# Kernel optimization log

Measured on AMD Instinct MI355X. Metric: run time of the kernel, lower is better.

The kernel has to match this reference:

```python
import jax, jax.numpy as jnp
import numpy as np
from math import factorial

N_SCALES = 4
K_ORI = 4
NA = 9


def _grids(h, w):
    fy = (jnp.arange(h) - h // 2) * (2.0 / h)
    fx = (jnp.arange(w) - w // 2) * (2.0 / w)
    FY, FX = jnp.meshgrid(fy, fx, indexing='ij')
    r = jnp.sqrt(FX ** 2 + FY ** 2)
    r = jnp.where(r == 0, 1.0 / max(h, w), r)
    return jnp.log2(r), jnp.arctan2(FY, FX)


def _rc_hi(lr, lo, hi):
    # sqrt raised-cosine rising 0->1 over log_rad in [lo, hi]
    t = jnp.clip((lr - lo) / (hi - lo), 0.0, 1.0)
    return jnp.sqrt(0.5 * (1.0 - jnp.cos(jnp.pi * t)))


def _rc_lo(lr, lo, hi):
    t = jnp.clip((lr - lo) / (hi - lo), 0.0, 1.0)
    return jnp.sqrt(0.5 * (1.0 + jnp.cos(jnp.pi * t)))


def _angle_masks(angle, K, is_complex):
    order = K - 1
    const = (2.0 ** (2 * order)) * (factorial(order) ** 2) / (K * factorial(2 * order))
    masks = []
    for b in range(K):
        d = jnp.mod(angle - jnp.pi * b / K + jnp.pi, 2 * jnp.pi) - jnp.pi
        if is_complex:  # single-sided (analytic) mask
            m = 2.0 * np.sqrt(const) * (jnp.cos(d) ** order) * (jnp.abs(d) < jnp.pi / 2)
        else:
            m = np.sqrt(const) * (jnp.cos(d) ** order)
        masks.append(m)
    return masks


def _build_pyramid(img, n_scales, K):
    # complex steerable pyramid in the frequency domain (tight_frame=False)
    order = K - 1
    h, w = img.shape
    imdft = jnp.fft.fftshift(jnp.fft.fft2(img))
    lr, ang = _grids(h, w)
    hi0 = _rc_hi(lr, -1.0, 0.0)
    lo0 = _rc_lo(lr, -1.0, 0.0)
    coeffs = {'residual_highpass': jnp.real(jnp.fft.ifft2(jnp.fft.ifftshift(imdft * hi0)))}
    lodft = imdft * lo0
    cph = (-1j) ** order
    for s in range(n_scales):
        hh, ww = lodft.shape
        lr, ang = _grids(hh, ww)
        him = _rc_hi(lr, -2.0, -1.0)
        for b, am in enumerate(_angle_masks(ang, K, True)):
            coeffs[(s, b)] = jnp.fft.ifft2(jnp.fft.ifftshift(cph * lodft * him * am))
        # spectral crop = spatial downsample by 2, then lowpass
        lodft = lodft[hh // 4: hh // 4 + hh // 2, ww // 4: ww // 4 + ww // 2]
        lr2, _ = _grids(hh // 2, ww // 2)
        lodft = lodft * _rc_lo(lr2, -1.0, 0.0)
    coeffs['residual_lowpass'] = jnp.real(jnp.fft.ifft2(jnp.fft.ifftshift(lodft)))
    return coeffs


def _lo0_filter(im):
    # height-0 pyramid residual lowpass == lo0 filtering (filterPyr in the torch code)
    h, w = im.shape
    lr, _ = _grids(h, w)
    return jnp.real(jnp.fft.ifft2(jnp.fft.ifftshift(jnp.fft.fftshift(jnp.fft.fft2(im)) * _rc_lo(lr, -1.0, 0.0))))


def _expand(im, f=2):
    # frequency-domain upsampling by factor f (Portilla_Simoncelli.expand)
    h, w = im.shape
    dft = jnp.fft.fftshift(jnp.fft.fft2(im)).astype(jnp.complex64)
    big = jnp.zeros((f * h, f * w), dtype=jnp.complex64)
    big = big.at[(f * h - h) // 2:(f * h - h) // 2 + h, (f * w - w) // 2:(f * w - w) // 2 + w].set(dft)
    return jnp.fft.ifft2(jnp.fft.ifftshift(big)) * (f * f)


def _recon_band(real_bands, K):
    # recon_pyr(levels=[0]) of a height-1 real pyramid whose bands were replaced
    order = K - 1
    h, w = real_bands[0].shape
    lr, ang = _grids(h, w)
    lo0 = _rc_lo(lr, -1.0, 0.0)
    him = _rc_hi(lr, -2.0, -1.0)
    ph = (1j) ** order
    recondft = jnp.zeros((h, w), dtype=jnp.complex64)
    for b, am in enumerate(_angle_masks(ang, K, False)):
        recondft = recondft + ph * jnp.fft.fftshift(jnp.fft.fft2(real_bands[b])) * him * am
    return jnp.real(jnp.fft.ifft2(jnp.fft.ifftshift(recondft * lo0)))


def _autocorr(ch, la):
    h, w = ch.shape
    F = jnp.fft.fft2(ch)
    ac = jnp.fft.fftshift(jnp.real(jnp.fft.ifft2(jnp.abs(F) ** 2))) / (h * w)
    cx, cy = h // 2, w // 2
    le = int(min(min(h, w) / 2 - 1, la))
    return ac[cx - le:cx + le + 1, cy - le:cy + le + 1], ac[cx, cy], le


def _skew_kurt(ch, vari, var0):
    cond = (vari / var0) > 1e-6
    skew = jnp.where(cond, jnp.mean(ch ** 3) / (vari ** 1.5), 0.0)
    kurt = jnp.where(cond, jnp.mean(ch ** 4) / (vari ** 2), 3.0)
    return skew, kurt


def _ps_forward(image):
    n_scales, K, Na = N_SCALES, K_ORI, NA
    img = image.reshape(image.shape[-2], image.shape[-1])
    mu = jnp.mean(img)
    var0 = jnp.var(img, ddof=1)
    cimg = img - mu
    pix = jnp.stack([mu, var0,
                     jnp.mean(cimg ** 3) / (var0 ** 1.5),
                     jnp.mean(cimg ** 4) / (var0 ** 2),
                     jnp.min(img), jnp.max(img)])
    coeffs = _build_pyramid(img, n_scales, K)
    coeffs['residual_lowpass'] = coeffs['residual_lowpass'] - jnp.mean(coeffs['residual_lowpass'])
    keys = ['residual_highpass'] + [(s, b) for s in range(n_scales) for b in range(K)] + ['residual_lowpass']
    mag, realc, mag_means = {}, {}, []
    for kk in keys:
        v = coeffs[kk]
        m = jnp.abs(v)
        mm = jnp.mean(m)
        mag_means.append(mm)
        mag[kk] = m - mm
        realc[kk] = jnp.real(v)
    mag_means = jnp.stack(mag_means)
    la = (Na - 1) // 2
    auto_corr = jnp.zeros((Na, Na, n_scales + 1))
    acm = jnp.zeros((Na, Na, n_scales, K))
    skew_r = jnp.zeros((n_scales + 1,))
    kurt_r = jnp.zeros((n_scales + 1,))
    recon = _lo0_filter(coeffs['residual_lowpass'])
    patch, vari, le = _autocorr(recon, la)
    auto_corr = auto_corr.at[la - le:la + le + 1, la - le:la + le + 1, n_scales].set(patch)
    sk, ku = _skew_kurt(recon, vari, var0)
    skew_r = skew_r.at[n_scales].set(sk)
    kurt_r = kurt_r.at[n_scales].set(ku)
    for s in range(n_scales - 1, -1, -1):
        for b in range(K):
            patch, vari, le = _autocorr(mag[(s, b)], la)
            acm = acm.at[la - le:la + le + 1, la - le:la + le + 1, s, b].set(patch)
        recon = jnp.real(_expand(recon, 2) / 4.0)
        recon = recon + _recon_band([realc[(s, b)] for b in range(K)], K)
        patch, vari, le = _autocorr(recon, la)
        auto_corr = auto_corr.at[la - le:la + le + 1, la - le:la + le + 1, s].set(patch)
        sk, ku = _skew_kurt(recon, vari, var0)
        skew_r = skew_r.at[s].set(sk)
        kurt_r = kurt_r.at[s].set(ku)
    K2 = max(2 * K, 5)
    coc_mag = jnp.zeros((K, K, n_scales + 1))
    csc_mag = jnp.zeros((K, K, n_scales))
    coc_real = jnp.zeros((K2, K2, n_scales + 1))
    csc_real = jnp.zeros((2 * K, K2, n_scales))
    for s in range(n_scales):
        hs, ws = realc[(s, 0)].shape
        csz = hs * ws
        if s < n_scales - 1:
            pars, rpr, rpi = [], [], []
            for b in range(K):
                tmp = _expand(coeffs[(s + 1, b)], 2) / 4.0
                rt, it = jnp.real(tmp), jnp.imag(tmp)
                mg = jnp.sqrt(rt ** 2 + it ** 2)
                a2 = 2.0 * jnp.arctan2(rt, it)  # note arg order matches torch code
                rpr.append((mg * jnp.cos(a2)).T.reshape(-1))
                rpi.append((mg * jnp.sin(a2)).T.reshape(-1))
                pars.append((mg - jnp.mean(mg)).T.reshape(-1))
            parents = jnp.stack(pars, 1)
            rparents = jnp.stack(rpr + rpi, 1)
        else:
            tmp = jnp.real(_expand(coeffs['residual_lowpass'], 2) / 4.0).T
            rparents = jnp.stack([tmp.reshape(-1),
                                  jnp.roll(tmp, 1, 0).reshape(-1),
                                  jnp.roll(tmp, -1, 0).reshape(-1),
                                  jnp.roll(tmp, 1, 1).reshape(-1),
                                  jnp.roll(tmp, -1, 1).reshape(-1)], 1)
            parents = None
        cousins = jnp.stack([mag[(s, b)].T.reshape(-1) for b in range(K)], 1)
        coc_mag = coc_mag.at[:, :, s].set(cousins.T @ cousins / csz)
        if parents is not None:
            csc_mag = csc_mag.at[:, :, s].set(cousins.T @ parents / csz)
        rcousins = jnp.stack([realc[(s, b)].T.reshape(-1) for b in range(K)], 1)
        coc_real = coc_real.at[:K, :K, s].set(rcousins.T @ rcousins / csz)
        nrp = rparents.shape[1]
        csc_real = csc_real.at[:K, :nrp, s].set(rcousins.T @ rparents / csz)
        if s == n_scales - 1:
            coc_real = coc_real.at[:nrp, :nrp, n_scales].set(rparents.T @ rparents / (csz / 4.0))
    var_hp = jnp.mean(coeffs['residual_highpass'] ** 2)
    return jnp.concatenate([pix, mag_means, acm.reshape(-1), skew_r, kurt_r,
                            auto_corr.reshape(-1), coc_mag.reshape(-1), csc_mag.reshape(-1),
                            coc_real.reshape(-1), csc_real.reshape(-1), var_hp.reshape(1)])


def setup_inputs() -> dict:
    key = jax.random.key(0)
    image = jax.random.normal(key, (1, 1, 1024, 1024), dtype=jnp.float32)
    return {"image": image}


def reference(image):
    return _ps_forward(image)
```

## Files before the change

### kernel.cpp

```cpp
#include <hip/hip_runtime.h>
#include <math.h>

typedef float2 cplx;

#define PI_F 3.14159265358979323846f
#define SQC  0.8944271909999159f

#define GS_FOR(i, n) for (int i = blockIdx.x * blockDim.x + threadIdx.x; i < (n); i += gridDim.x * blockDim.x)
#define RED_GRID 256

__device__ __forceinline__ float ufreq(int i, int n) {
  return (float)((i < (n >> 1)) ? i : i - n) * (2.0f / (float)n);
}
__device__ __forceinline__ void grid_lr_ang(int i, int j, int n, float* lr, float* ang) {
  float fy = ufreq(i, n), fx = ufreq(j, n);
  float r = sqrtf(fx * fx + fy * fy);
  if (i == 0 && j == 0) r = 1.0f / (float)n;
  *lr = log2f(r);
  *ang = atan2f(fy, fx);
}
__device__ __forceinline__ float rc_hi_f(float lr, float lo, float hi) {
  float t = (lr - lo) / (hi - lo);
  t = fminf(fmaxf(t, 0.0f), 1.0f);
  return sqrtf(0.5f * (1.0f - cosf(PI_F * t)));
}
__device__ __forceinline__ float rc_lo_f(float lr, float lo, float hi) {
  float t = (lr - lo) / (hi - lo);
  t = fminf(fmaxf(t, 0.0f), 1.0f);
  return sqrtf(0.5f * (1.0f + cosf(PI_F * t)));
}
__device__ __forceinline__ float wrap_d(float ang, int b) {
  float d = ang - PI_F * (float)b * 0.25f + PI_F;
  d = d - floorf(d * (0.5f / PI_F)) * (2.0f * PI_F);
  return d - PI_F;
}
__device__ __forceinline__ float amask_c(float ang, int b) {
  float d = wrap_d(ang, b);
  float c = cosf(d);
  float m = 2.0f * SQC * c * c * c;
  return (fabsf(d) < 0.5f * PI_F) ? m : 0.0f;
}
__device__ __forceinline__ float amask_r(float ang, int b) {
  float d = wrap_d(ang, b);
  float c = cosf(d);
  return SQC * c * c * c;
}

__device__ __forceinline__ double wred_d(double v) {
#pragma unroll
  for (int o = 32; o > 0; o >>= 1) v += __shfl_down(v, o);
  return v;
}
template<int NS>
__device__ __forceinline__ void block_to_parts(double* __restrict__ part, int slotBase, double* v) {
  __shared__ double lds[NS][4];
  const int wid = threadIdx.x >> 6, lane = threadIdx.x & 63;
#pragma unroll
  for (int q = 0; q < NS; ++q) {
    double r = wred_d(v[q]);
    if (lane == 0) lds[q][wid] = r;
  }
  __syncthreads();
  for (int q = threadIdx.x; q < NS; q += blockDim.x) {
    double s = lds[q][0] + lds[q][1] + lds[q][2] + lds[q][3];
    part[(size_t)(slotBase + q) * RED_GRID + blockIdx.x] = s;
  }
}
__global__ void reduce_parts_k(double* __restrict__ acc, const double* __restrict__ part, int base) {
  const double* p = part + (size_t)(base + blockIdx.x) * RED_GRID;
  double s = 0;
  for (int i = threadIdx.x; i < RED_GRID; i += 64) s += p[i];
  s = wred_d(s);
  if (threadIdx.x == 0) acc[base + blockIdx.x] = s;
}
__device__ __forceinline__ void atomicMinF(float* a, float v) {
  if (v >= 0.0f) atomicMin((int*)a, __float_as_int(v));
  else atomicMax((unsigned int*)a, __float_as_uint(v));
}
__device__ __forceinline__ void atomicMaxF(float* a, float v) {
  if (v >= 0.0f) atomicMax((int*)a, __float_as_int(v));
  else atomicMin((unsigned int*)a, __float_as_uint(v));
}

template<int LOGN, bool INV>
__global__ __launch_bounds__(256) void fft_rows_k(cplx* __restrict__ d) {
  constexpr int N = 1 << LOGN;
  __shared__ cplx sh[N];
  __shared__ cplx tw[N / 2];
  const int tid = threadIdx.x;
  const int T = blockDim.x;
  cplx* rp = d + (size_t)blockIdx.x * N;
  for (int k = tid; k < N / 2; k += T) {
    float a = (INV ? 2.0f : -2.0f) * PI_F * (float)k / (float)N;
    float s, c;
    sincosf(a, &s, &c);
    tw[k] = make_float2(c, s);
  }
  for (int i = tid; i < N; i += T) {
    unsigned r = __brev((unsigned)i) >> (32 - LOGN);
    sh[r] = rp[i];
  }
  __syncthreads();
  for (int len = 2; len <= N; len <<= 1) {
    const int half = len >> 1;
    const int tstep = N / len;
    for (int j = tid; j < N / 2; j += T) {
      int pos = j & (half - 1);
      int base = (j - pos) << 1;
      cplx w = tw[pos * tstep];
      cplx a = sh[base + pos];
      cplx b = sh[base + pos + half];
      float tx = b.x * w.x - b.y * w.y;
      float ty = b.x * w.y + b.y * w.x;
      sh[base + pos] = make_float2(a.x + tx, a.y + ty);
      sh[base + pos + half] = make_float2(a.x - tx, a.y - ty);
    }
    __syncthreads();
  }
  const float sc = INV ? (1.0f / (float)N) : 1.0f;
  for (int i = tid; i < N; i += T) {
    cplx v = sh[i];
    rp[i] = make_float2(v.x * sc, v.y * sc);
  }
}

__global__ void transpose_k(cplx* __restrict__ out, const cplx* __restrict__ in, int N) {
  __shared__ cplx tile[32][33];
  size_t po = (size_t)blockIdx.z * N * N;
  int bx = blockIdx.x * 32, by = blockIdx.y * 32;
  int x = bx + threadIdx.x;
  for (int dy = threadIdx.y; dy < 32; dy += 8)
    tile[dy][threadIdx.x] = in[po + (size_t)(by + dy) * N + x];
  __syncthreads();
  int xo = by + threadIdx.x;
  for (int dy = threadIdx.y; dy < 32; dy += 8)
    out[po + (size_t)(bx + dy) * N + xo] = tile[threadIdx.x][dy];
}

__global__ void r2c_k(cplx* out, const float* in, int n) {
  GS_FOR(i, n) out[i] = make_float2(in[i], 0.0f);
}
__global__ void hp_lo_split_k(cplx* hp, cplx* lod, const cplx* spec, int logN) {
  int N = 1 << logN, n = N * N;
  GS_FOR(idx, n) {
    int i = idx >> logN, j = idx & (N - 1);
    float lr, ang;
    grid_lr_ang(i, j, N, &lr, &ang);
    float h0 = rc_hi_f(lr, -1.0f, 0.0f);
    float l0 = rc_lo_f(lr, -1.0f, 0.0f);
    cplx z = spec[idx];
    hp[idx]  = make_float2(z.x * h0, z.y * h0);
    lod[idx] = make_float2(z.x * l0, z.y * l0);
  }
}
__global__ void rhp_stats_k(const cplx* src, int n, double* part) {
  double sa = 0, sq = 0;
  GS_FOR(i, n) {
    float v = src[i].x;
    sa += fabsf(v);
    sq += (double)v * (double)v;
  }
  double v[2] = {sa, sq};
  block_to_parts<2>(part, 4, v);
}
__global__ void band_spec_k(cplx* out, const cplx* lod, int logN, int b0, int P) {
  int N = 1 << logN, n = N * N;
  GS_FOR(idx, n) {
    int i = idx >> logN, j = idx & (N - 1);
    float lr, ang;
    grid_lr_ang(i, j, N, &lr, &ang);
    float him = rc_hi_f(lr, -2.0f, -1.0f);
    cplx z = lod[idx];
    for (int p = 0; p < P; ++p) {
      float m = him * amask_c(ang, b0 + p);
      out[p * n + idx] = make_float2(-z.y * m, z.x * m);
    }
  }
}
template<int P>
__global__ void extract_band_k(float* realc, float* mag, const cplx* src, int logPer,
                               double* part, int slotBase) {
  int n = (1 << logPer) * P;
  double s0 = 0, s1 = 0, s2 = 0, s3 = 0;
  GS_FOR(idx, n) {
    cplx z = src[idx];
    float m = sqrtf(z.x * z.x + z.y * z.y);
    realc[idx] = z.x;
    mag[idx] = m;
    int p = idx >> logPer;
    if (p == 0) s0 += m; else if (p == 1) s1 += m; else if (p == 2) s2 += m; else s3 += m;
  }
  double v[4] = {s0, s1, s2, s3};
  block_to_parts<P>(part, slotBase, v);
}
__global__ void center_k(float* buf, int logPer, int P, const double* acc0) {
  int nPer = 1 << logPer, n = nPer * P;
  double inv = 1.0 / (double)nPer;
  GS_FOR(idx, n) buf[idx] -= (float)(acc0[idx >> logPer] * inv);
}
__global__ void lod_down_k(cplx* child, const cplx* par, int logNc) {
  int Nc = 1 << logNc, n = Nc * Nc, Np = Nc << 1;
  GS_FOR(idx, n) {
    int i = idx >> logNc, j = idx & (Nc - 1);
    int pi = (i < (Nc >> 1)) ? i : i + Nc;
    int pj = (j < (Nc >> 1)) ? j : j + Nc;
    float lr, ang;
    grid_lr_ang(i, j, Nc, &lr, &ang);
    float l0 = rc_lo_f(lr, -1.0f, 0.0f);
    cplx z = par[pi * Np + pj];
    child[idx] = make_float2(z.x * l0, z.y * l0);
  }
}
__global__ void sum_real2_k(const cplx* src, int n, double* part) {
  double s = 0;
  GS_FOR(i, n) s += (double)src[i].x;
  double v[1] = {s};
  block_to_parts<1>(part, 24, v);
}
__global__ void center_abs2_k(const cplx* src, int n, const double* acc, double* part) {
  float mu = (float)(acc[24] / (double)n);
  double s = 0;
  GS_FOR(i, n) s += fabsf(src[i].x - mu);
  double v[1] = {s};
  block_to_parts<1>(part, 25, v);
}
__global__ void rs4_init_k(cplx* rs, const cplx* lod4) {
  GS_FOR(idx, 4096) {
    int i = idx >> 6, j = idx & 63;
    float lr, ang;
    grid_lr_ang(i, j, 64, &lr, &ang);
    float l0 = rc_lo_f(lr, -1.0f, 0.0f);
    cplx v = lod4[idx];
    if (idx == 0) v = make_float2(0.0f, 0.0f);
    rs[idx] = make_float2(v.x * l0, v.y * l0);
  }
}
__global__ void embed_rs_k(cplx* dst, const cplx* src, int logNb, int zeroDC) {
  int Nb = 1 << logNb, Nc = Nb >> 1, q = Nc >> 1, n = Nb * Nb;
  GS_FOR(idx, n) {
    int i = idx >> logNb, j = idx & (Nb - 1);
    int ci = (i < q) ? i : ((i >= Nb - q) ? (i - Nb + Nc) : -1);
    int cj = (j < q) ? j : ((j >= Nb - q) ? (j - Nb + Nc) : -1);
    cplx v = make_float2(0.0f, 0.0f);
    if (ci >= 0 && cj >= 0) {
      v = src[ci * Nc + cj];
      if (zeroDC && ci == 0 && cj == 0) v = make_float2(0.0f, 0.0f);
    }
    dst[idx] = v;
  }
}
__global__ void recon_step_k(cplx* __restrict__ dst, const cplx* __restrict__ src,
                             const cplx* __restrict__ lod, int logNb) {
  int Nb = 1 << logNb, Nc = Nb >> 1, qq = Nc >> 1, n = Nb * Nb;
  GS_FOR(idx, n) {
    int i = idx >> logNb, j = idx & (Nb - 1);
    int ci = (i < qq) ? i : ((i >= Nb - qq) ? (i - Nb + Nc) : -1);
    int cj = (j < qq) ? j : ((j >= Nb - qq) ? (j - Nb + Nc) : -1);
    float ex = 0.0f, ey = 0.0f;
    if (ci >= 0 && cj >= 0) { cplx v = src[ci * Nc + cj]; ex = v.x; ey = v.y; }
    int ni = (Nb - i) & (Nb - 1), nj = (Nb - j) & (Nb - 1);
    float lr, ang;
    grid_lr_ang(i, j, Nb, &lr, &ang);
    float him = rc_hi_f(lr, -2.0f, -1.0f);
    float l0 = rc_lo_f(lr, -1.0f, 0.0f);
    cplx L = lod[idx];
    cplx L2 = lod[ni * Nb + nj];
    float sx = 0.0f, sy = 0.0f;
#pragma unroll
    for (int b = 0; b < 4; ++b) {
      float c1 = him * amask_c(ang, b);
      float c2 = him * amask_c(ang + PI_F, b);
      float mr = him * amask_r(ang, b);
      float gx = L.x * c1 - L2.x * c2;
      float gy = L.y * c1 + L2.y * c2;
      sx += 0.5f * mr * gx;
      sy += 0.5f * mr * gy;
    }
    dst[idx] = make_float2(ex + sx * l0, ey + sy * l0);
  }
}
__global__ void embed_band_k(cplx* dst, const cplx* lodc, int logNb, int b0, int P) {
  int Nb = 1 << logNb, Nc = Nb >> 1, q = Nc >> 1, n = Nb * Nb;
  int tot = n * P;
  GS_FOR(idxAll, tot) {
    int p = idxAll >> (2 * logNb);
    int idx = idxAll & (n - 1);
    int i = idx >> logNb, j = idx & (Nb - 1);
    int ci = (i < q) ? i : ((i >= Nb - q) ? (i - Nb + Nc) : -1);
    int cj = (j < q) ? j : ((j >= Nb - q) ? (j - Nb + Nc) : -1);
    cplx v = make_float2(0.0f, 0.0f);
    if (ci >= 0 && cj >= 0) {
      float lr, ang;
      grid_lr_ang(ci, cj, Nc, &lr, &ang);
      float m = rc_hi_f(lr, -2.0f, -1.0f) * amask_c(ang, b0 + p);
      cplx z = lodc[ci * Nc + cj];
      v = make_float2(-z.y * m, z.x * m);
    }
    dst[idxAll] = v;
  }
}
template<int ST, bool SK>
__device__ __forceinline__ void ac_core(const float* __restrict__ xp, int logN,
                                        double* __restrict__ part, int slotBase) {
  const int N = 1 << logN;
  const int nu = (N * N) >> 3;
  float acc[41];
#pragma unroll
  for (int q = 0; q < 41; ++q) acc[q] = 0.0f;
  float a3 = 0.0f, a4 = 0.0f;
  for (int u = blockIdx.x * blockDim.x + threadIdx.x; u < nu; u += gridDim.x * blockDim.x) {
    int i = u >> (logN - 3);
    int j0 = (u & ((N >> 3) - 1)) << 3;
    float buf[5][16];
#pragma unroll
    for (int di = 0; di < 5; ++di) {
      int r = ((i + di) & (N - 1)) << logN;
#pragma unroll
      for (int blk = 0; blk < 4; ++blk) {
        int c = (j0 - 4 + blk * 4) & (N - 1);
        if (ST == 1) {
          const float4 v = *reinterpret_cast<const float4*>(xp + r + c);
          buf[di][blk * 4 + 0] = v.x; buf[di][blk * 4 + 1] = v.y;
          buf[di][blk * 4 + 2] = v.z; buf[di][blk * 4 + 3] = v.w;
        } else {
          const float4 v0 = *reinterpret_cast<const float4*>(xp + ((size_t)(r + c) << 1));
          const float4 v1 = *reinterpret_cast<const float4*>(xp + ((size_t)(r + c) << 1) + 4);
          buf[di][blk * 4 + 0] = v0.x; buf[di][blk * 4 + 1] = v0.z;
          buf[di][blk * 4 + 2] = v1.x; buf[di][blk * 4 + 3] = v1.z;
        }
      }
    }
#pragma unroll
    for (int k = 0; k < 8; ++k) {
      float xc = buf[0][4 + k];
      if (SK) {
        float x2 = xc * xc;
        a3 += x2 * xc;
        a4 += x2 * x2;
      }
#pragma unroll
      for (int q = 0; q < 41; ++q) {
        const int di = (q < 5) ? 0 : 1 + (q - 5) / 9;
        const int dj = (q < 5) ? q : ((q - 5) % 9) - 4;
        acc[q] += xc * buf[di][4 + k + dj];
      }
    }
  }
  constexpr int NS = SK ? 43 : 41;
  double v[NS];
#pragma unroll
  for (int q = 0; q < 41; ++q) v[q] = (double)acc[q];
  if (SK) { v[41] = (double)a3; v[42] = (double)a4; }
  block_to_parts<NS>(part, slotBase, v);
}
__global__ __launch_bounds__(256) void acm_vec_k(const float* m0, const float* m1,
                                                 const float* m2, const float* m3, double* part) {
  const int s = blockIdx.z;
  const float* base = (s == 0) ? m0 : ((s == 1) ? m1 : ((s == 2) ? m2 : m3));
  const int logN = 10 - s;
  const float* xp = base + ((size_t)blockIdx.y << (2 * logN));
  ac_core<1, false>(xp, logN, part, 448 + (s * 4 + blockIdx.y) * 41);
}
__global__ __launch_bounds__(256) void ac_rec_k(const float* x, int logN, double* part, int slotBase) {
  ac_core<2, true>(x, logN, part, slotBase);
}
__global__ void img_stats1_k(const float* img, int n, double* part, float* mm) {
  double s = 0;
  float mn = INFINITY, mx = -INFINITY;
  GS_FOR(i, n) {
    float v = img[i];
    s += (double)v;
    mn = fminf(mn, v);
    mx = fmaxf(mx, v);
  }
  double v[1] = {s};
  block_to_parts<1>(part, 0, v);
#pragma unroll
  for (int o = 32; o > 0; o >>= 1) {
    mn = fminf(mn, __shfl_down(mn, o));
    mx = fmaxf(mx, __shfl_down(mx, o));
  }
  if ((threadIdx.x & 63) == 0) {
    atomicMinF(mm + 0, mn);
    atomicMaxF(mm + 1, mx);
  }
}
__global__ void img_stats2_k(const float* img, int n, const double* acc, double* part) {
  double mu = acc[0] / (double)n;
  double s2 = 0, s3 = 0, s4 = 0;
  GS_FOR(i, n) {
    double c = (double)img[i] - mu;
    double c2 = c * c;
    s2 += c2;
    s3 += c2 * c;
    s4 += c2 * c2;
  }
  double v[3] = {s2, s3, s4};
  block_to_parts<3>(part, 1, v);
}
template<bool WS>
__global__ void gram4_k(const float* base, int n, double* part, int slotBase) {
  constexpr int NS = WS ? 20 : 16;
  double g[16];
  double s[4];
#pragma unroll
  for (int q = 0; q < 16; ++q) g[q] = 0;
#pragma unroll
  for (int q = 0; q < 4; ++q) s[q] = 0;
  GS_FOR(i, n) {
    double d0 = base[i], d1 = base[n + i], d2 = base[2 * n + i], d3 = base[3 * n + i];
    g[0] += d0 * d0; g[1] += d0 * d1; g[2]  += d0 * d2; g[3]  += d0 * d3;
    g[5] += d1 * d1; g[6] += d1 * d2; g[7]  += d1 * d3;
    g[10] += d2 * d2; g[11] += d2 * d3;
    g[15] += d3 * d3;
    if (WS) { s[0] += d0; s[1] += d1; s[2] += d2; s[3] += d3; }
  }
  g[4] = g[1]; g[8] = g[2]; g[12] = g[3]; g[9] = g[6]; g[13] = g[7]; g[14] = g[11];
  double v[NS];
#pragma unroll
  for (int q = 0; q < 16; ++q) v[q] = g[q];
  if (WS) {
#pragma unroll
    for (int q = 0; q < 4; ++q) v[16 + q] = s[q];
  }
  block_to_parts<NS>(part, slotBase, v);
}
__global__ void parent_reduce_k(const cplx* par, const float* magS, const float* realS, int n,
                                double* part, int slotBase) {
  double d[13];
#pragma unroll
  for (int q = 0; q < 13; ++q) d[q] = 0;
  GS_FOR(i, n) {
    cplx z = par[i];
    float rt = z.x, it = z.y;
    float mg = sqrtf(rt * rt + it * it);
    float rpr = 0.0f, rpi = 0.0f;
    if (mg > 0.0f) {
      rpr = (it * it - rt * rt) / mg;
      rpi = 2.0f * rt * it / mg;
    }
    d[0] += (double)mg;
#pragma unroll
    for (int b = 0; b < 4; ++b) d[1 + b] += (double)magS[b * n + i] * (double)mg;
#pragma unroll
    for (int b = 0; b < 4; ++b) {
      double rv = (double)realS[b * n + i];
      d[5 + b] += rv * (double)rpr;
      d[9 + b] += rv * (double)rpi;
    }
  }
  block_to_parts<13>(part, slotBase, d);
}
__global__ void lp_parent2_k(const cplx* X, const float* realS, int logN, double* part) {
  int N = 1 << logN, n = N * N;
  double d[45];
#pragma unroll
  for (int q = 0; q < 45; ++q) d[q] = 0;
  GS_FOR(idx, n) {
    int i = idx >> logN, j = idx & (N - 1);
    float c[5];
    c[0] = X[idx].x;
    c[1] = X[i * N + ((j - 1) & (N - 1))].x;
    c[2] = X[i * N + ((j + 1) & (N - 1))].x;
    c[3] = X[((i - 1) & (N - 1)) * N + j].x;
    c[4] = X[((i + 1) & (N - 1)) * N + j].x;
#pragma unroll
    for (int b = 0; b < 4; ++b) {
      double rv = (double)realS[b * n + idx];
#pragma unroll
      for (int k = 0; k < 5; ++k) d[b * 5 + k] += rv * (double)c[k];
    }
#pragma unroll
    for (int a = 0; a < 5; ++a)
#pragma unroll
      for (int k = 0; k < 5; ++k) d[20 + a * 5 + k] += (double)c[a] * (double)c[k];
  }
  block_to_parts<45>(part, 370, d);
}
__global__ void init_mm_k(float* mm) {
  if (threadIdx.x == 0) { mm[0] = INFINITY; mm[1] = -INFINITY; }
}

__global__ void assemble_k(float* out, const double* acc, const float* mm) {
  const int t = threadIdx.x;
  const double NPIX = 1048576.0;
  double var0 = acc[1] / (NPIX - 1.0);
  if (t == 0) {
    double mu = acc[0] / NPIX;
    out[0] = (float)mu;
    out[1] = (float)var0;
    out[2] = (float)((acc[2] / NPIX) / pow(var0, 1.5));
    out[3] = (float)((acc[3] / NPIX) / (var0 * var0));
    out[4] = mm[0];
    out[5] = mm[1];
    out[2455] = (float)(acc[5] / NPIX);
  }
  for (int k = t; k < 18; k += blockDim.x) {
    double n, sv;
    if (k == 0) { n = NPIX; sv = acc[4]; }
    else if (k == 17) { n = 4096.0; sv = acc[25]; }
    else { int s = (k - 1) >> 2; double dd = (double)(1024 >> s); n = dd * dd; sv = acc[7 + k]; }
    out[6 + k] = (float)(sv / n);
  }
  for (int si = t; si < 5; si += blockDim.x) {
    double dd = (si == 4) ? 64.0 : (double)(1024 >> si);
    double nn = dd * dd;
    double vari = acc[1104 + si * 43] / nn;
    bool cond = (vari / var0) > 1e-6;
    double m3 = acc[1104 + si * 43 + 41] / nn, m4 = acc[1104 + si * 43 + 42] / nn;
    out[1320 + si] = (float)(cond ? m3 / pow(vari, 1.5) : 0.0);
    out[1325 + si] = (float)(cond ? m4 / (vari * vari) : 3.0);
  }
  for (int w = t; w < 656; w += blockDim.x) {
    int patch = w / 41, q = w - patch * 41;
    int s = patch >> 2, b = patch & 3;
    double dd = (double)(1024 >> s);
    double v = acc[448 + w] / (dd * dd);
    int di = (q < 5) ? 0 : 1 + (q - 5) / 9;
    int dj = (q < 5) ? q : ((q - 5) % 9) - 4;
    int pi = 4 + di, pj = 4 + dj;
    out[24 + 144 * pi + 16 * pj + 4 * s + b] = (float)v;
    if (q) out[24 + 144 * (8 - pi) + 16 * (8 - pj) + 4 * s + b] = (float)v;
  }
  for (int w = t; w < 205; w += blockDim.x) {
    int si = w / 41, q = w - si * 41;
    double dd = (si == 4) ? 64.0 : (double)(1024 >> si);
    double v = acc[1104 + si * 43 + q] / (dd * dd);
    int di = (q < 5) ? 0 : 1 + (q - 5) / 9;
    int dj = (q < 5) ? q : ((q - 5) % 9) - 4;
    int pi = 4 + di, pj = 4 + dj;
    out[1330 + (pi * 9 + pj) * 5 + si] = (float)v;
    if (q) out[1330 + ((8 - pi) * 9 + (8 - pj)) * 5 + si] = (float)v;
  }
  for (int q = t; q < 64; q += blockDim.x) {
    int s = q >> 4, ij = q & 15;
    double dd = (double)(1024 >> s); double csz = dd * dd;
    out[1735 + ij * 5 + s] = (float)(acc[64 + s * 20 + ij] / csz);
  }
  for (int q = t; q < 64; q += blockDim.x) {
    int s = q >> 4, ij = q & 15;
    int i = ij >> 2, j = ij & 3;
    double dd = (double)(1024 >> s); double csz = dd * dd;
    out[1879 + (i * 8 + j) * 5 + s] = (float)(acc[144 + s * 16 + ij] / csz);
  }
  for (int q = t; q < 25; q += blockDim.x) {
    int a = q / 5, b2 = q - a * 5;
    out[1879 + (a * 8 + b2) * 5 + 4] = (float)(acc[390 + q] / 4096.0);
  }
  for (int q = t; q < 48; q += blockDim.x) {
    int s = q >> 4, ij = q & 15;
    int i = ij >> 2, pb = ij & 3;
    double dd = (double)(1024 >> s); double csz = dd * dd;
    const double* ps = acc + 208 + (s * 4 + pb) * 13;
    double meanp = ps[0] / csz;
    double cousSum = acc[64 + s * 20 + 16 + i];
    out[1815 + (i * 4 + pb) * 4 + s] = (float)((ps[1 + i] - meanp * cousSum) / csz);
  }
  for (int q = t; q < 96; q += blockDim.x) {
    int s = q >> 5, r = q & 31;
    int i = r >> 3, j = r & 7;
    int pb = j & 3, offq = (j >= 4) ? 9 : 5;
    double dd = (double)(1024 >> s); double csz = dd * dd;
    out[2199 + (i * 8 + j) * 4 + s] = (float)(acc[208 + (s * 4 + pb) * 13 + offq + i] / csz);
  }
  for (int q = t; q < 20; q += blockDim.x) {
    int i = q / 5, c = q - i * 5;
    out[2199 + (i * 8 + c) * 4 + 3] = (float)(acc[370 + q] / 16384.0);
  }
}

static void fft_rows(cplx* d, int N, int rows, bool inv, hipStream_t st) {
  dim3 g(rows);
  int T = (N >= 512) ? 256 : ((N == 256) ? 128 : 64);
  dim3 b(T);
  switch (N) {
    case 64:   if (inv) fft_rows_k<6,  true><<<g, b, 0, st>>>(d); else fft_rows_k<6,  false><<<g, b, 0, st>>>(d); break;
    case 128:  if (inv) fft_rows_k<7,  true><<<g, b, 0, st>>>(d); else fft_rows_k<7,  false><<<g, b, 0, st>>>(d); break;
    case 256:  if (inv) fft_rows_k<8,  true><<<g, b, 0, st>>>(d); else fft_rows_k<8,  false><<<g, b, 0, st>>>(d); break;
    case 512:  if (inv) fft_rows_k<9,  true><<<g, b, 0, st>>>(d); else fft_rows_k<9,  false><<<g, b, 0, st>>>(d); break;
    case 1024: if (inv) fft_rows_k<10, true><<<g, b, 0, st>>>(d); else fft_rows_k<10, false><<<g, b, 0, st>>>(d); break;
    default: break;
  }
}
static void fft2d(cplx* a, cplx* b, int N, int P, bool inv, hipStream_t st) {
  fft_rows(a, N, N * P, inv, st);
  dim3 tg(N / 32, N / 32, P), tb(32, 8);
  transpose_k<<<tg, tb, 0, st>>>(b, a, N);
  fft_rows(b, N, N * P, inv, st);
  transpose_k<<<tg, tb, 0, st>>>(a, b, N);
}
static inline dim3 gsz(int n) {
  int b = (n + 255) >> 8;
  if (b > 2048) b = 2048;
  if (b < 1) b = 1;
  return dim3(b);
}

extern "C" void kernel_launch(void* const* d_in, const int* in_sizes, int n_in,
                              void* d_out, int out_size, void* d_ws, size_t ws_size,
                              hipStream_t stream) {
  (void)in_sizes; (void)n_in; (void)out_size; (void)ws_size;
  const float* img = (const float*)d_in[0];
  float* out = (float*)d_out;

  char* wsb = (char*)d_ws;
  size_t off = 0;
  auto alloc = [&](size_t bytes) -> void* {
    void* p = wsb + off;
    off += (bytes + 255) & ~(size_t)255;
    return p;
  };
  const size_t MB = (size_t)1 << 20;
  const int NSLOT = 1320;
  cplx* cA = (cplx*)alloc(16 * MB);
  cplx* cB = (cplx*)alloc(16 * MB);
  cplx* LOD[5];
  for (int s = 0; s < 5; ++s) {
    int N = 1024 >> s;
    LOD[s] = (cplx*)alloc((size_t)N * N * sizeof(cplx));
  }
  cplx* RS[4];
  for (int k = 0; k < 4; ++k) {
    int N = 64 << k;
    RS[k] = (cplx*)alloc((size_t)N * N * sizeof(cplx));
  }
  float* MAG[4];
  float* REALC[4];
  for (int s = 0; s < 4; ++s) {
    int N = 1024 >> s;
    MAG[s] = (float*)alloc((size_t)4 * N * N * sizeof(float));
  }
  for (int s = 0; s < 4; ++s) {
    int N = 1024 >> s;
    REALC[s] = (float*)alloc((size_t)4 * N * N * sizeof(float));
  }
  const int NPIX = 1024 * 1024;
  double* PART = (double*)alloc((size_t)NSLOT * RED_GRID * 8);
  double* ACC  = (double*)alloc(2048 * 8);
  float* MM    = (float*)alloc(256);

  auto finish = [&](int base, int count) {
    reduce_parts_k<<<dim3(count), 64, 0, stream>>>(ACC, PART, base);
  };

  hipMemsetAsync(out, 0, 2456 * sizeof(float), stream);
  init_mm_k<<<1, 64, 0, stream>>>(MM);

  img_stats1_k<<<dim3(RED_GRID), 256, 0, stream>>>(img, NPIX, PART, MM);
  finish(0, 1);
  img_stats2_k<<<dim3(RED_GRID), 256, 0, stream>>>(img, NPIX, ACC, PART);

  r2c_k<<<gsz(NPIX), 256, 0, stream>>>(cA, img, NPIX);
  fft2d(cA, cB, 1024, 1, false, stream);
  hp_lo_split_k<<<gsz(NPIX), 256, 0, stream>>>(cA, LOD[0], cA, 10);
  fft2d(cA, cB, 1024, 1, true, stream);
  rhp_stats_k<<<dim3(RED_GRID), 256, 0, stream>>>(cA, NPIX, PART);
  for (int b0 = 0; b0 < 4; b0 += 2) {
    band_spec_k<<<gsz(NPIX), 256, 0, stream>>>(cA, LOD[0], 10, b0, 2);
    fft2d(cA, cB, 1024, 2, true, stream);
    extract_band_k<2><<<dim3(RED_GRID), 256, 0, stream>>>(REALC[0] + (size_t)b0 * NPIX,
                                                          MAG[0] + (size_t)b0 * NPIX, cA, 20, PART, 8 + b0);
  }
  finish(8, 4);
  center_k<<<gsz(4 * NPIX), 256, 0, stream>>>(MAG[0], 20, 4, ACC + 8);
  lod_down_k<<<gsz(512 * 512), 256, 0, stream>>>(LOD[1], LOD[0], 9);
  for (int s = 1; s <= 3; ++s) {
    int N = 1024 >> s, logN = 10 - s, n = N * N;
    band_spec_k<<<gsz(n), 256, 0, stream>>>(cA, LOD[s], logN, 0, 4);
    fft2d(cA, cB, N, 4, true, stream);
    extract_band_k<4><<<dim3(RED_GRID), 256, 0, stream>>>(REALC[s], MAG[s], cA, 2 * logN, PART, 8 + 4 * s);
    finish(8 + 4 * s, 4);
    center_k<<<gsz(4 * n), 256, 0, stream>>>(MAG[s], 2 * logN, 4, ACC + 8 + 4 * s);
    lod_down_k<<<gsz((N / 2) * (N / 2)), 256, 0, stream>>>(LOD[s + 1], LOD[s], logN - 1);
  }
  hipMemcpyAsync(cA, LOD[4], 4096 * sizeof(cplx), hipMemcpyDeviceToDevice, stream);
  fft2d(cA, cB, 64, 1, true, stream);
  sum_real2_k<<<dim3(RED_GRID), 256, 0, stream>>>(cA, 4096, PART);
  finish(24, 1);
  center_abs2_k<<<dim3(RED_GRID), 256, 0, stream>>>(cA, 4096, ACC, PART);

  acm_vec_k<<<dim3(RED_GRID, 4, 4), 256, 0, stream>>>(MAG[0], MAG[1], MAG[2], MAG[3], PART);

  rs4_init_k<<<gsz(4096), 256, 0, stream>>>(RS[0], LOD[4]);
  hipMemcpyAsync(cA, RS[0], 4096 * sizeof(cplx), hipMemcpyDeviceToDevice, stream);
  fft2d(cA, cB, 64, 1, true, stream);
  ac_rec_k<<<dim3(RED_GRID), 256, 0, stream>>>((const float*)cA, 6, PART, 1104 + 4 * 43);
  cplx* cur = RS[0];
  for (int s = 3; s >= 0; --s) {
    int N = 1024 >> s, logN = 10 - s, n = N * N;
    cplx* nxt = (s > 0) ? RS[4 - s] : cA;
    recon_step_k<<<gsz(n), 256, 0, stream>>>(nxt, cur, LOD[s], logN);
    if (s > 0) {
      hipMemcpyAsync(cA, nxt, (size_t)n * sizeof(cplx), hipMemcpyDeviceToDevice, stream);
    }
    fft2d(cA, cB, N, 1, true, stream);
    ac_rec_k<<<dim3(RED_GRID), 256, 0, stream>>>((const float*)cA, logN, PART, 1104 + s * 43);
    cur = nxt;
  }

  for (int s = 0; s < 4; ++s) {
    int n = (1024 >> s) * (1024 >> s);
    gram4_k<true><<<dim3(RED_GRID), 256, 0, stream>>>(MAG[s], n, PART, 64 + s * 20);
    gram4_k<false><<<dim3(RED_GRID), 256, 0, stream>>>(REALC[s], n, PART, 144 + s * 16);
  }
  for (int pb0 = 0; pb0 < 4; pb0 += 2) {
    embed_band_k<<<gsz(2 * NPIX), 256, 0, stream>>>(cA, LOD[1], 10, pb0, 2);
    fft2d(cA, cB, 1024, 2, true, stream);
    for (int p = 0; p < 2; ++p)
      parent_reduce_k<<<dim3(RED_GRID), 256, 0, stream>>>(cA + (size_t)p * NPIX, MAG[0], REALC[0], NPIX,
                                                          PART, 208 + (pb0 + p) * 13);
  }
  for (int s = 1; s <= 2; ++s) {
    int N = 1024 >> s, logN = 10 - s, n = N * N;
    embed_band_k<<<gsz(4 * n), 256, 0, stream>>>(cA, LOD[s + 1], logN, 0, 4);
    fft2d(cA, cB, N, 4, true, stream);
    for (int p = 0; p < 4; ++p)
      parent_reduce_k<<<dim3(RED_GRID), 256, 0, stream>>>(cA + (size_t)p * n, MAG[s], REALC[s], n,
                                                          PART, 208 + (s * 4 + p) * 13);
  }
  embed_rs_k<<<gsz(128 * 128), 256, 0, stream>>>(cA, LOD[4], 7, 1);
  fft2d(cA, cB, 128, 1, true, stream);
  lp_parent2_k<<<dim3(RED_GRID), 256, 0, stream>>>(cA, REALC[3], 7, PART);

  finish(0, NSLOT);
  assemble_k<<<1, 256, 0, stream>>>(out, ACC, MM);
}
```

Baseline: 1.216 ms.

## Fuse spectrum masking into FFT row loads and drop the final transpose in inverse FFTs

The row-FFT kernel now takes a load mode, so it can build its input on the fly: real-to-complex promotion, the highpass mask, band masks and the embedded upsampled band spectra. This removes the separate mask and embed kernels and several device memcpys. Inverse 2-D FFTs now skip the final transpose and return transposed output, and the downstream index conventions are swapped to match (neighbour offsets in parent_reduce and the pi/pj mapping in assemble). It saves several full passes over the 1024x1024 complex buffers, but the fused loads recompute masks per FFT row and rely on the transposed-layout index fixes being correct throughout.

```diff
diff --git a/kernel.cpp b/kernel.cpp
--- a/kernel.cpp
+++ b/kernel.cpp
@@ -8,6 +8,12 @@
 
 #define GS_FOR(i, n) for (int i = blockIdx.x * blockDim.x + threadIdx.x; i < (n); i += gridDim.x * blockDim.x)
 #define RED_GRID 256
+
+#define MD_PLAIN 0
+#define MD_R2C   1
+#define MD_HP    2
+#define MD_BAND  3
+#define MD_EMB   4
 
 __device__ __forceinline__ float ufreq(int i, int n) {
   return (float)((i < (n >> 1)) ? i : i - n) * (2.0f / (float)n);
@@ -82,23 +88,56 @@
   else atomicMin((unsigned int*)a, __float_as_uint(v));
 }
 
-template<int LOGN, bool INV>
-__global__ __launch_bounds__(256) void fft_rows_k(cplx* __restrict__ d) {
+template<int LOGN, bool INV, int MODE>
+__global__ __launch_bounds__(256) void fftm_k(cplx* __restrict__ dst, const void* __restrict__ srcv,
+                                              const cplx* __restrict__ aux, int b0) {
   constexpr int N = 1 << LOGN;
   __shared__ cplx sh[N];
   __shared__ cplx tw[N / 2];
   const int tid = threadIdx.x;
   const int T = blockDim.x;
-  cplx* rp = d + (size_t)blockIdx.x * N;
+  const int r = blockIdx.x;
+  const int i = r & (N - 1);
+  const int p = r >> LOGN;
   for (int k = tid; k < N / 2; k += T) {
     float a = (INV ? 2.0f : -2.0f) * PI_F * (float)k / (float)N;
     float s, c;
     sincosf(a, &s, &c);
     tw[k] = make_float2(c, s);
   }
-  for (int i = tid; i < N; i += T) {
-    unsigned r = __brev((unsigned)i) >> (32 - LOGN);
-    sh[r] = rp[i];
+  for (int j = tid; j < N; j += T) {
+    cplx v;
+    if (MODE == MD_PLAIN) {
+      v = ((const cplx*)srcv)[(size_t)r * N + j];
+    } else if (MODE == MD_R2C) {
+      v = make_float2(((const float*)srcv)[(size_t)r * N + j], 0.0f);
+    } else if (MODE == MD_HP) {
+      v = ((const cplx*)srcv)[(size_t)r * N + j];
+      float lr, ang;
+      grid_lr_ang(i, j, N, &lr, &ang);
+      float h0 = rc_hi_f(lr, -1.0f, 0.0f);
+      v.x *= h0; v.y *= h0;
+    } else if (MODE == MD_BAND) {
+      float lr, ang;
+      grid_lr_ang(i, j, N, &lr, &ang);
+      float m = rc_hi_f(lr, -2.0f, -1.0f) * amask_c(ang, b0 + p);
+      cplx z = aux[i * N + j];
+      v = make_float2(-z.y * m, z.x * m);
+    } else {
+      const int Nc = N >> 1, q = Nc >> 1;
+      int ci = (i < q) ? i : ((i >= N - q) ? (i - N + Nc) : -1);
+      int cj = (j < q) ? j : ((j >= N - q) ? (j - N + Nc) : -1);
+      v = make_float2(0.0f, 0.0f);
+      if (ci >= 0 && cj >= 0) {
+        float lr, ang;
+        grid_lr_ang(ci, cj, Nc, &lr, &ang);
+        float m = rc_hi_f(lr, -2.0f, -1.0f) * amask_c(ang, b0 + p);
+        cplx z = aux[ci * Nc + cj];
+        v = make_float2(-z.y * m, z.x * m);
+      }
+    }
+    unsigned rr = __brev((unsigned)j) >> (32 - LOGN);
+    sh[rr] = v;
   }
   __syncthreads();
   for (int len = 2; len <= N; len <<= 1) {
@@ -118,9 +157,9 @@
     __syncthreads();
   }
   const float sc = INV ? (1.0f / (float)N) : 1.0f;
-  for (int i = tid; i < N; i += T) {
-    cplx v = sh[i];
-    rp[i] = make_float2(v.x * sc, v.y * sc);
+  for (int j = tid; j < N; j += T) {
+    cplx v = sh[j];
+    dst[(size_t)r * N + j] = make_float2(v.x * sc, v.y * sc);
   }
 }
 
@@ -137,19 +176,14 @@
     out[po + (size_t)(bx + dy) * N + xo] = tile[threadIdx.x][dy];
 }
 
-__global__ void r2c_k(cplx* out, const float* in, int n) {
-  GS_FOR(i, n) out[i] = make_float2(in[i], 0.0f);
-}
-__global__ void hp_lo_split_k(cplx* hp, cplx* lod, const cplx* spec, int logN) {
+__global__ void lod_only_k(cplx* lod, const cplx* spec, int logN) {
   int N = 1 << logN, n = N * N;
   GS_FOR(idx, n) {
     int i = idx >> logN, j = idx & (N - 1);
     float lr, ang;
     grid_lr_ang(i, j, N, &lr, &ang);
-    float h0 = rc_hi_f(lr, -1.0f, 0.0f);
     float l0 = rc_lo_f(lr, -1.0f, 0.0f);
     cplx z = spec[idx];
-    hp[idx]  = make_float2(z.x * h0, z.y * h0);
     lod[idx] = make_float2(z.x * l0, z.y * l0);
   }
 }
@@ -162,20 +196,6 @@
   }
   double v[2] = {sa, sq};
   block_to_parts<2>(part, 4, v);
-}
-__global__ void band_spec_k(cplx* out, const cplx* lod, int logN, int b0, int P) {
-  int N = 1 << logN, n = N * N;
-  GS_FOR(idx, n) {
-    int i = idx >> logN, j = idx & (N - 1);
-    float lr, ang;
-    grid_lr_ang(i, j, N, &lr, &ang);
-    float him = rc_hi_f(lr, -2.0f, -1.0f);
-    cplx z = lod[idx];
-    for (int p = 0; p < P; ++p) {
-      float m = him * amask_c(ang, b0 + p);
-      out[p * n + idx] = make_float2(-z.y * m, z.x * m);
-    }
-  }
 }
 template<int P>
 __global__ void extract_band_k(float* realc, float* mag, const cplx* src, int logPer,
@@ -279,26 +299,6 @@
     dst[idx] = make_float2(ex + sx * l0, ey + sy * l0);
   }
 }
-__global__ void embed_band_k(cplx* dst, const cplx* lodc, int logNb, int b0, int P) {
-  int Nb = 1 << logNb, Nc = Nb >> 1, q = Nc >> 1, n = Nb * Nb;
-  int tot = n * P;
-  GS_FOR(idxAll, tot) {
-    int p = idxAll >> (2 * logNb);
-    int idx = idxAll & (n - 1);
-    int i = idx >> logNb, j = idx & (Nb - 1);
-    int ci = (i < q) ? i : ((i >= Nb - q) ? (i - Nb + Nc) : -1);
-    int cj = (j < q) ? j : ((j >= Nb - q) ? (j - Nb + Nc) : -1);
-    cplx v = make_float2(0.0f, 0.0f);
-    if (ci >= 0 && cj >= 0) {
-      float lr, ang;
-      grid_lr_ang(ci, cj, Nc, &lr, &ang);
-      float m = rc_hi_f(lr, -2.0f, -1.0f) * amask_c(ang, b0 + p);
-      cplx z = lodc[ci * Nc + cj];
-      v = make_float2(-z.y * m, z.x * m);
-    }
-    dst[idxAll] = v;
-  }
-}
 template<int ST, bool SK>
 __device__ __forceinline__ void ac_core(const float* __restrict__ xp, int logN,
                                         double* __restrict__ part, int slotBase) {
@@ -460,10 +460,10 @@
     int i = idx >> logN, j = idx & (N - 1);
     float c[5];
     c[0] = X[idx].x;
-    c[1] = X[i * N + ((j - 1) & (N - 1))].x;
-    c[2] = X[i * N + ((j + 1) & (N - 1))].x;
-    c[3] = X[((i - 1) & (N - 1)) * N + j].x;
-    c[4] = X[((i + 1) & (N - 1)) * N + j].x;
+    c[1] = X[((i - 1) & (N - 1)) * N + j].x;
+    c[2] = X[((i + 1) & (N - 1)) * N + j].x;
+    c[3] = X[i * N + ((j - 1) & (N - 1))].x;
+    c[4] = X[i * N + ((j + 1) & (N - 1))].x;
 #pragma unroll
     for (int b = 0; b < 4; ++b) {
       double rv = (double)realS[b * n + idx];
@@ -518,7 +518,7 @@
     double v = acc[448 + w] / (dd * dd);
     int di = (q < 5) ? 0 : 1 + (q - 5) / 9;
     int dj = (q < 5) ? q : ((q - 5) % 9) - 4;
-    int pi = 4 + di, pj = 4 + dj;
+    int pi = 4 + dj, pj = 4 + di;
     out[24 + 144 * pi + 16 * pj + 4 * s + b] = (float)v;
     if (q) out[24 + 144 * (8 - pi) + 16 * (8 - pj) + 4 * s + b] = (float)v;
   }
@@ -528,7 +528,7 @@
     double v = acc[1104 + si * 43 + q] / (dd * dd);
     int di = (q < 5) ? 0 : 1 + (q - 5) / 9;
     int dj = (q < 5) ? q : ((q - 5) % 9) - 4;
-    int pi = 4 + di, pj = 4 + dj;
+    int pi = 4 + dj, pj = 4 + di;
     out[1330 + (pi * 9 + pj) * 5 + si] = (float)v;
     if (q) out[1330 + ((8 - pi) * 9 + (8 - pj)) * 5 + si] = (float)v;
   }
@@ -569,25 +569,45 @@
   }
 }
 
-static void fft_rows(cplx* d, int N, int rows, bool inv, hipStream_t st) {
-  dim3 g(rows);
-  int T = (N >= 512) ? 256 : ((N == 256) ? 128 : 64);
-  dim3 b(T);
+static inline int thr_for(int N) { return (N >= 512) ? 256 : ((N == 256) ? 128 : 64); }
+template<int MODE>
+static void fft_pass(int N, int rows, bool inv, cplx* dst, const void* src, const cplx* aux,
+                     int b0, hipStream_t st) {
+  dim3 g(rows), b(thr_for(N));
   switch (N) {
-    case 64:   if (inv) fft_rows_k<6,  true><<<g, b, 0, st>>>(d); else fft_rows_k<6,  false><<<g, b, 0, st>>>(d); break;
-    case 128:  if (inv) fft_rows_k<7,  true><<<g, b, 0, st>>>(d); else fft_rows_k<7,  false><<<g, b, 0, st>>>(d); break;
-    case 256:  if (inv) fft_rows_k<8,  true><<<g, b, 0, st>>>(d); else fft_rows_k<8,  false><<<g, b, 0, st>>>(d); break;
-    case 512:  if (inv) fft_rows_k<9,  true><<<g, b, 0, st>>>(d); else fft_rows_k<9,  false><<<g, b, 0, st>>>(d); break;
-    case 1024: if (inv) fft_rows_k<10, true><<<g, b, 0, st>>>(d); else fft_rows_k<10, false><<<g, b, 0, st>>>(d); break;
+    case 64:
+      if (inv) fftm_k<6, true, MODE><<<g, b, 0, st>>>(dst, src, aux, b0);
+      else     fftm_k<6, false, MODE><<<g, b, 0, st>>>(dst, src, aux, b0);
+      break;
+    case 128:
+      if (inv) fftm_k<7, true, MODE><<<g, b, 0, st>>>(dst, src, aux, b0);
+      else     fftm_k<7, false, MODE><<<g, b, 0, st>>>(dst, src, aux, b0);
+      break;
+    case 256:
+      if (inv) fftm_k<8, true, MODE><<<g, b, 0, st>>>(dst, src, aux, b0);
+      else     fftm_k<8, false, MODE><<<g, b, 0, st>>>(dst, src, aux, b0);
+      break;
+    case 512:
+      if (inv) fftm_k<9, true, MODE><<<g, b, 0, st>>>(dst, src, aux, b0);
+      else     fftm_k<9, false, MODE><<<g, b, 0, st>>>(dst, src, aux, b0);
+      break;
+    case 1024:
+      if (inv) fftm_k<10, true, MODE><<<g, b, 0, st>>>(dst, src, aux, b0);
+      else     fftm_k<10, false, MODE><<<g, b, 0, st>>>(dst, src, aux, b0);
+      break;
     default: break;
   }
 }
-static void fft2d(cplx* a, cplx* b, int N, int P, bool inv, hipStream_t st) {
-  fft_rows(a, N, N * P, inv, st);
+static void transp(cplx* out, const cplx* in, int N, int P, hipStream_t st) {
   dim3 tg(N / 32, N / 32, P), tb(32, 8);
-  transpose_k<<<tg, tb, 0, st>>>(b, a, N);
-  fft_rows(b, N, N * P, inv, st);
-  transpose_k<<<tg, tb, 0, st>>>(a, b, N);
+  transpose_k<<<tg, tb, 0, st>>>(out, in, N);
+}
+template<int MODE>
+static void ifft2dT(int N, int P, cplx* out, cplx* tmp, const void* src, const cplx* aux,
+                    int b0, hipStream_t st) {
+  fft_pass<MODE>(N, N * P, true, tmp, src, aux, b0, st);
+  transp(out, tmp, N, P, st);
+  fft_pass<MD_PLAIN>(N, N * P, true, out, out, nullptr, 0, st);
 }
 static inline dim3 gsz(int n) {
   int b = (n + 255) >> 8;
@@ -650,52 +670,47 @@
   finish(0, 1);
   img_stats2_k<<<dim3(RED_GRID), 256, 0, stream>>>(img, NPIX, ACC, PART);
 
-  r2c_k<<<gsz(NPIX), 256, 0, stream>>>(cA, img, NPIX);
-  fft2d(cA, cB, 1024, 1, false, stream);
-  hp_lo_split_k<<<gsz(NPIX), 256, 0, stream>>>(cA, LOD[0], cA, 10);
-  fft2d(cA, cB, 1024, 1, true, stream);
+  fft_pass<MD_R2C>(1024, 1024, false, cA, img, nullptr, 0, stream);
+  transp(cB, cA, 1024, 1, stream);
+  fft_pass<MD_PLAIN>(1024, 1024, false, cB, cB, nullptr, 0, stream);
+  transp(cA, cB, 1024, 1, stream);
+  lod_only_k<<<gsz(NPIX), 256, 0, stream>>>(LOD[0], cA, 10);
+  ifft2dT<MD_HP>(1024, 1, cA, cB, cA, nullptr, 0, stream);
   rhp_stats_k<<<dim3(RED_GRID), 256, 0, stream>>>(cA, NPIX, PART);
   for (int b0 = 0; b0 < 4; b0 += 2) {
-    band_spec_k<<<gsz(NPIX), 256, 0, stream>>>(cA, LOD[0], 10, b0, 2);
-    fft2d(cA, cB, 1024, 2, true, stream);
+    ifft2dT<MD_BAND>(1024, 2, cB, cA, nullptr, LOD[0], b0, stream);
     extract_band_k<2><<<dim3(RED_GRID), 256, 0, stream>>>(REALC[0] + (size_t)b0 * NPIX,
-                                                          MAG[0] + (size_t)b0 * NPIX, cA, 20, PART, 8 + b0);
+                                                          MAG[0] + (size_t)b0 * NPIX, cB, 20, PART, 8 + b0);
   }
   finish(8, 4);
   center_k<<<gsz(4 * NPIX), 256, 0, stream>>>(MAG[0], 20, 4, ACC + 8);
   lod_down_k<<<gsz(512 * 512), 256, 0, stream>>>(LOD[1], LOD[0], 9);
   for (int s = 1; s <= 3; ++s) {
     int N = 1024 >> s, logN = 10 - s, n = N * N;
-    band_spec_k<<<gsz(n), 256, 0, stream>>>(cA, LOD[s], logN, 0, 4);
-    fft2d(cA, cB, N, 4, true, stream);
-    extract_band_k<4><<<dim3(RED_GRID), 256, 0, stream>>>(REALC[s], MAG[s], cA, 2 * logN, PART, 8 + 4 * s);
+    ifft2dT<MD_BAND>(N, 4, cB, cA, nullptr, LOD[s], 0, stream);
+    extract_band_k<4><<<dim3(RED_GRID), 256, 0, stream>>>(REALC[s], MAG[s], cB, 2 * logN, PART, 8 + 4 * s);
     finish(8 + 4 * s, 4);
     center_k<<<gsz(4 * n), 256, 0, stream>>>(MAG[s], 2 * logN, 4, ACC + 8 + 4 * s);
     lod_down_k<<<gsz((N / 2) * (N / 2)), 256, 0, stream>>>(LOD[s + 1], LOD[s], logN - 1);
   }
-  hipMemcpyAsync(cA, LOD[4], 4096 * sizeof(cplx), hipMemcpyDeviceToDevice, stream);
-  fft2d(cA, cB, 64, 1, true, stream);
-  sum_real2_k<<<dim3(RED_GRID), 256, 0, stream>>>(cA, 4096, PART);
+  ifft2dT<MD_PLAIN>(64, 1, cB, cA, LOD[4], nullptr, 0, stream);
+  sum_real2_k<<<dim3(RED_GRID), 256, 0, stream>>>(cB, 4096, PART);
   finish(24, 1);
-  center_abs2_k<<<dim3(RED_GRID), 256, 0, stream>>>(cA, 4096, ACC, PART);
+  center_abs2_k<<<dim3(RED_GRID), 256, 0, stream>>>(cB, 4096, ACC, PART);
 
   acm_vec_k<<<dim3(RED_GRID, 4, 4), 256, 0, stream>>>(MAG[0], MAG[1], MAG[2], MAG[3], PART);
 
   rs4_init_k<<<gsz(4096), 256, 0, stream>>>(RS[0], LOD[4]);
-  hipMemcpyAsync(cA, RS[0], 4096 * sizeof(cplx), hipMemcpyDeviceToDevice, stream);
-  fft2d(cA, cB, 64, 1, true, stream);
-  ac_rec_k<<<dim3(RED_GRID), 256, 0, stream>>>((const float*)cA, 6, PART, 1104 + 4 * 43);
+  ifft2dT<MD_PLAIN>(64, 1, cB, cA, RS[0], nullptr, 0, stream);
+  ac_rec_k<<<dim3(RED_GRID), 256, 0, stream>>>((const float*)cB, 6, PART, 1104 + 4 * 43);
   cplx* cur = RS[0];
   for (int s = 3; s >= 0; --s) {
     int N = 1024 >> s, logN = 10 - s, n = N * N;
-    cplx* nxt = (s > 0) ? RS[4 - s] : cA;
-    recon_step_k<<<gsz(n), 256, 0, stream>>>(nxt, cur, LOD[s], logN);
-    if (s > 0) {
-      hipMemcpyAsync(cA, nxt, (size_t)n * sizeof(cplx), hipMemcpyDeviceToDevice, stream);
-    }
-    fft2d(cA, cB, N, 1, true, stream);
-    ac_rec_k<<<dim3(RED_GRID), 256, 0, stream>>>((const float*)cA, logN, PART, 1104 + s * 43);
-    cur = nxt;
+    cplx* sp = (s > 0) ? RS[4 - s] : cB;
+    recon_step_k<<<gsz(n), 256, 0, stream>>>(sp, cur, LOD[s], logN);
+    ifft2dT<MD_PLAIN>(N, 1, cB, cA, sp, nullptr, 0, stream);
+    ac_rec_k<<<dim3(RED_GRID), 256, 0, stream>>>((const float*)cB, logN, PART, 1104 + s * 43);
+    cur = sp;
   }
 
   for (int s = 0; s < 4; ++s) {
@@ -704,23 +719,21 @@
     gram4_k<false><<<dim3(RED_GRID), 256, 0, stream>>>(REALC[s], n, PART, 144 + s * 16);
   }
   for (int pb0 = 0; pb0 < 4; pb0 += 2) {
-    embed_band_k<<<gsz(2 * NPIX), 256, 0, stream>>>(cA, LOD[1], 10, pb0, 2);
-    fft2d(cA, cB, 1024, 2, true, stream);
+    ifft2dT<MD_EMB>(1024, 2, cB, cA, nullptr, LOD[1], pb0, stream);
     for (int p = 0; p < 2; ++p)
-      parent_reduce_k<<<dim3(RED_GRID), 256, 0, stream>>>(cA + (size_t)p * NPIX, MAG[0], REALC[0], NPIX,
+      parent_reduce_k<<<dim3(RED_GRID), 256, 0, stream>>>(cB + (size_t)p * NPIX, MAG[0], REALC[0], NPIX,
                                                           PART, 208 + (pb0 + p) * 13);
   }
   for (int s = 1; s <= 2; ++s) {
-    int N = 1024 >> s, logN = 10 - s, n = N * N;
-    embed_band_k<<<gsz(4 * n), 256, 0, stream>>>(cA, LOD[s + 1], logN, 0, 4);
-    fft2d(cA, cB, N, 4, true, stream);
+    int N = 1024 >> s, n = N * N;
+    ifft2dT<MD_EMB>(N, 4, cB, cA, nullptr, LOD[s + 1], 0, stream);
     for (int p = 0; p < 4; ++p)
-      parent_reduce_k<<<dim3(RED_GRID), 256, 0, stream>>>(cA + (size_t)p * n, MAG[s], REALC[s], n,
+      parent_reduce_k<<<dim3(RED_GRID), 256, 0, stream>>>(cB + (size_t)p * n, MAG[s], REALC[s], n,
                                                           PART, 208 + (s * 4 + p) * 13);
   }
   embed_rs_k<<<gsz(128 * 128), 256, 0, stream>>>(cA, LOD[4], 7, 1);
-  fft2d(cA, cB, 128, 1, true, stream);
-  lp_parent2_k<<<dim3(RED_GRID), 256, 0, stream>>>(cA, REALC[3], 7, PART);
+  ifft2dT<MD_PLAIN>(128, 1, cB, cA + 16384, cA, nullptr, 0, stream);
+  lp_parent2_k<<<dim3(RED_GRID), 256, 0, stream>>>(cB, REALC[3], 7, PART);
 
   finish(0, NSLOT);
   assemble_k<<<1, 256, 0, stream>>>(out, ACC, MM);
```

Measured after the change: 1.152 ms. 5.3% less time.
